# Kernel optimization log

Measured on AMD Instinct MI355X. Metric: run time of the kernel, lower is better.

The kernel has to match this reference:

```python
import jax, jax.numpy as jnp
import numpy as np

EPS = 1e-06  # used both as eps and as the F.threshold threshold (mqjs passes eps as th)


def _pair_log_dist_sum(x1, x2, th):
    # dist[i,j] = ||x1_i||^2 + ||x2_j||^2 - 2 x1_i . x2_j  (n x n)
    x1x2 = x1 @ x2.T
    sq1 = jnp.sum(x1 * x1, axis=1)[:, None]
    sq2 = jnp.sum(x2 * x2, axis=1)[None, :]
    dist = sq1 + sq2 - 2.0 * x1x2
    # F.threshold(dist, th, 1): values <= th -> 1; then clamp(min=1), sqrt, log, row-sum
    dist = jnp.where(dist > th, dist, 1.0)
    dist = jnp.maximum(dist, 1.0)
    return jnp.sum(0.5 * jnp.log(dist), axis=1)  # log(sqrt(d)) == 0.5*log(d)


def _mqjs(inp, tgt, eps):
    n = inp.shape[0]
    x1 = inp.reshape(n, -1)
    x2 = tgt.reshape(n, -1)
    p = (x1 + x2) / 2.0
    ce = _pair_log_dist_sum(x1, p, eps) + _pair_log_dist_sum(x2, p, eps)
    se = _pair_log_dist_sum(x1, x1, eps) * (n / (n - 1))
    return jnp.mean(ce - se)


def setup_inputs() -> dict:
    key = jax.random.key(0)
    k1, k2 = jax.random.split(key)
    n, d = 8192, 256
    inp = jax.random.normal(k1, (n, d), dtype=jnp.float32)
    tgt = jax.random.normal(k2, (n, d), dtype=jnp.float32)
    return {"input": inp, "target": tgt}


def reference(input, target):
    return _mqjs(input, target, EPS)
```

## Files before the change

kernel.cpp:

```cpp
#include <hip/hip_runtime.h>

#define N 8192
#define D 256
#define BM 128
#define BJ 64
#define JG 8
#define GJ (N / BJ / JG)
#define GI (N / BM)
#define NPART (3 * GI * GJ)

typedef int   i32x4 __attribute__((ext_vector_type(4)));
typedef int   i32x8 __attribute__((ext_vector_type(8)));
typedef float f32x4 __attribute__((ext_vector_type(4)));
typedef float f32x2 __attribute__((ext_vector_type(2)));

__device__ __forceinline__ unsigned pack_fp8x4(float a, float b, float c, float d) {
    unsigned lo = __builtin_amdgcn_cvt_pk_fp8_f32(a, b, 0, false);
    return __builtin_amdgcn_cvt_pk_fp8_f32(c, d, lo, true);
}
__device__ __forceinline__ float dequant_sumsq(unsigned q) {
    const float v0 = __builtin_amdgcn_cvt_f32_fp8(q, 0);
    const float v1 = __builtin_amdgcn_cvt_f32_fp8(q, 1);
    const float v2 = __builtin_amdgcn_cvt_f32_fp8(q, 2);
    const float v3 = __builtin_amdgcn_cvt_f32_fp8(q, 3);
    return fmaf(v0, v0, fmaf(v1, v1, fmaf(v2, v2, v3 * v3)));
}

__global__ void prep_kernel(const float* __restrict__ x1, const float* __restrict__ x2,
                            unsigned* __restrict__ x1q, unsigned* __restrict__ x2q,
                            unsigned* __restrict__ pq,
                            float* __restrict__ sq1, float* __restrict__ sq2,
                            float* __restrict__ sqp) {
    const int tid = threadIdx.x, lane = tid & 63, wv = tid >> 6;
    const int row = blockIdx.x * 4 + wv;
    const size_t eb = (size_t)row * D + lane * 4;
    const float4 a = *(const float4*)(x1 + eb);
    const float4 b = *(const float4*)(x2 + eb);
    const float px = 0.5f * (a.x + b.x), py = 0.5f * (a.y + b.y);
    const float pz = 0.5f * (a.z + b.z), pw = 0.5f * (a.w + b.w);
    const unsigned qa = pack_fp8x4(a.x, a.y, a.z, a.w);
    const unsigned qb = pack_fp8x4(b.x, b.y, b.z, b.w);
    const unsigned qp = pack_fp8x4(px, py, pz, pw);
    const size_t wb = (size_t)row * (D / 4) + lane;
    x1q[wb] = qa; x2q[wb] = qb; pq[wb] = qp;
    float s1 = dequant_sumsq(qa), s2 = dequant_sumsq(qb), sp = dequant_sumsq(qp);
    #pragma unroll
    for (int o = 32; o > 0; o >>= 1) {
        s1 += __shfl_down(s1, o, 64);
        s2 += __shfl_down(s2, o, 64);
        sp += __shfl_down(sp, o, 64);
    }
    if (lane == 0) { sq1[row] = s1; sq2[row] = s2; sqp[row] = sp; }
}

__device__ __forceinline__ f32x4 mfma8(i32x8 a, i32x8 b, f32x4 c) {
    return __builtin_amdgcn_mfma_scale_f32_16x16x128_f8f6f4(
        a, b, c, 0, 0, 0, 0x7F7F7F7F, 0, 0x7F7F7F7F);
}

__device__ __forceinline__ i32x8 read_frag(const unsigned char* Ts, int m, int quad) {
    const int r7 = m & 7;
    const i32x4 lo = *(const i32x4*)(Ts + m * 128 + ((((2 * quad)     ^ r7)) << 4));
    const i32x4 hi = *(const i32x4*)(Ts + m * 128 + ((((2 * quad + 1) ^ r7)) << 4));
    i32x8 f;
    f[0] = lo[0]; f[1] = lo[1]; f[2] = lo[2]; f[3] = lo[3];
    f[4] = hi[0]; f[5] = hi[1]; f[6] = hi[2]; f[7] = hi[3];
    return f;
}

__device__ __forceinline__ void stageB8(const unsigned char* __restrict__ g,
                                        unsigned char* s, int rowbase, size_t kb,
                                        int wv, int srow, int sblk) {
    const int row = wv * 8 + srow;
    __builtin_amdgcn_global_load_lds(
        (const __attribute__((address_space(1))) void*)(g + (size_t)(rowbase + row) * D + kb + sblk * 16),
        (__attribute__((address_space(3))) void*)(s + wv * 1024), 16, 0, 0);
}

__device__ __forceinline__ float logsumP(const f32x4 (&acc)[2][2],
                                         const f32x2 (&sa01)[2], const f32x2 (&sa23)[2],
                                         const float sb[2]) {
    float s = 0.0f;
    #pragma unroll
    for (int ti = 0; ti < 2; ++ti) {
        f32x2 pr = {1.0f, 1.0f};
        #pragma unroll
        for (int tj = 0; tj < 2; ++tj) {
            const f32x2 sbv = {sb[tj], sb[tj]};
            const f32x2 t01 = sa01[ti] + sbv, t23 = sa23[ti] + sbv;
            const f32x2 v01 = {acc[ti][tj][0], acc[ti][tj][1]};
            const f32x2 v23 = {acc[ti][tj][2], acc[ti][tj][3]};
            f32x2 d01 = t01 - 2.0f * v01;
            f32x2 d23 = t23 - 2.0f * v23;
            d01 = __builtin_elementwise_max(d01, (f32x2){1.0f, 1.0f});
            d23 = __builtin_elementwise_max(d23, (f32x2){1.0f, 1.0f});
            pr *= d01; pr *= d23;
        }
        s += __log2f(pr.x * pr.y);
    }
    return s;
}

__device__ __forceinline__ float logsumStraddle(const f32x4 (&acc)[2][2],
                                                const f32x2 (&sa01)[2], const f32x2 (&sa23)[2],
                                                const float sb[2],
                                                int wr, int wc, int quad, int l15,
                                                int I0, int J0) {
    float s = 0.0f;
    #pragma unroll
    for (int ti = 0; ti < 2; ++ti) {
        #pragma unroll
        for (int tj = 0; tj < 2; ++tj) {
            const int j = J0 + wc * 32 + tj * 16 + l15;
            float pr = 1.0f;
            #pragma unroll
            for (int r = 0; r < 4; ++r) {
                const int i = I0 + wr * 32 + ti * 16 + quad * 4 + r;
                const float sav = (r < 2) ? ((r & 1) ? sa01[ti].y : sa01[ti].x)
                                          : ((r & 1) ? sa23[ti].y : sa23[ti].x);
                float d = fmaf(-2.0f, acc[ti][tj][r], sav + sb[tj]);
                d = fmaxf(d, 1.0f);
                const float t = (j > i) ? d : 1.0f;
                const float u = (j >= i) ? d : 1.0f;
                pr *= t * u;
            }
            s += __log2f(pr);
        }
    }
    return s;
}

__global__ __launch_bounds__(512, 4) void mqjs_main(
    const unsigned char* __restrict__ x1q, const unsigned char* __restrict__ x2q,
    const unsigned char* __restrict__ pq,
    const float* __restrict__ sq1, const float* __restrict__ sq2,
    const float* __restrict__ sqp, float* __restrict__ partials) {

    __shared__ __align__(16) unsigned char Bs[3][2 * BJ * 128];
    __shared__ float red[8];

    const int tid = threadIdx.x;
    const int lane = tid & 63;
    const int wv = tid >> 6;
    const int wr = wv >> 1, wc = wv & 1;
    const int quad = lane >> 4, l15 = lane & 15;
    const int srow = lane >> 3;
    const int sblk = (lane & 7) ^ srow;

    const int z = blockIdx.z;
    const int I0 = blockIdx.y * BM;
    const int jbase = blockIdx.x * JG;
    const int pid = (z * GI + blockIdx.y) * GJ + blockIdx.x;
    const float wse = -(float)N / (float)(N - 1);

    int jj0 = 0;
    if (z == 2) {
        jj0 = 2 * (int)blockIdx.y - jbase;
        if (jj0 < 0) jj0 = 0;
        if (jj0 >= JG) { if (tid == 0) partials[pid] = 0.0f; return; }
    }

    const unsigned char* Ag = (z == 1) ? x2q : x1q;
    const unsigned char* Bg = (z == 2) ? x1q : pq;
    const float* sqAg = (z == 1) ? sq2 : sq1;
    const float* sqBg = (z == 2) ? sq1 : sqp;

    i32x8 af[2][2];
    f32x2 sa01[2], sa23[2];
    #pragma unroll
    for (int ti = 0; ti < 2; ++ti) {
        #pragma unroll
        for (int kc = 0; kc < 2; ++kc) {
            const size_t ro = (size_t)(I0 + wr * 32 + ti * 16 + l15) * D + kc * 128 + quad * 32;
            af[kc][ti] = *(const i32x8*)(Ag + ro);
        }
        const int sbase = I0 + wr * 32 + ti * 16 + quad * 4;
        const float4 sv = *(const float4*)(sqAg + sbase);
        sa01[ti] = (f32x2){sv.x, sv.y};
        sa23[ti] = (f32x2){sv.z, sv.w};
    }

    stageB8(Bg, Bs[0],        (jbase + jj0) * BJ, 0,   wv, srow, sblk);
    stageB8(Bg, Bs[0] + 8192, (jbase + jj0) * BJ, 128, wv, srow, sblk);
    if (jj0 + 1 < JG) {
        stageB8(Bg, Bs[1],        (jbase + jj0 + 1) * BJ, 0,   wv, srow, sblk);
        stageB8(Bg, Bs[1] + 8192, (jbase + jj0 + 1) * BJ, 128, wv, srow, sblk);
    }

    float tsum = 0.0f;
    const f32x4 zero4 = {0.0f, 0.0f, 0.0f, 0.0f};
    int cur = 0;

    for (int jj = jj0; jj < JG; ++jj) {
        const int J0 = (jbase + jj) * BJ;

        if (jj + 1 < JG) asm volatile("s_waitcnt vmcnt(2)" ::: "memory");
        else             asm volatile("s_waitcnt vmcnt(0)" ::: "memory");
        asm volatile("s_barrier" ::: "memory");

        float sb[2];
        sb[0] = sqBg[J0 + wc * 32 + l15];
        sb[1] = sqBg[J0 + wc * 32 + 16 + l15];

        if (jj + 2 < JG) {
            const int b2 = (cur == 0) ? 2 : cur - 1;
            stageB8(Bg, Bs[b2],        (jbase + jj + 2) * BJ, 0,   wv, srow, sblk);
            stageB8(Bg, Bs[b2] + 8192, (jbase + jj + 2) * BJ, 128, wv, srow, sblk);
        }

        i32x8 bfr0[2], bfr1[2];
        #pragma unroll
        for (int tj = 0; tj < 2; ++tj) {
            bfr0[tj] = read_frag(Bs[cur],        wc * 32 + tj * 16 + l15, quad);
            bfr1[tj] = read_frag(Bs[cur] + 8192, wc * 32 + tj * 16 + l15, quad);
        }

        f32x4 acc[2][2];
        __builtin_amdgcn_s_setprio(1);
        #pragma unroll
        for (int ti = 0; ti < 2; ++ti)
            #pragma unroll
            for (int tj = 0; tj < 2; ++tj)
                acc[ti][tj] = mfma8(af[0][ti], bfr0[tj], zero4);
        #pragma unroll
        for (int ti = 0; ti < 2; ++ti)
            #pragma unroll
            for (int tj = 0; tj < 2; ++tj)
                acc[ti][tj] = mfma8(af[1][ti], bfr1[tj], acc[ti][tj]);
        __builtin_amdgcn_s_setprio(0);

        if (z < 2) {
            tsum += 0.5f * logsumP(acc, sa01, sa23, sb);
        } else if (J0 >= I0 + BM) {
            tsum += wse * logsumP(acc, sa01, sa23, sb);
        } else {
            tsum += 0.5f * wse * logsumStraddle(acc, sa01, sa23, sb, wr, wc, quad, l15, I0, J0);
        }

        cur = (cur == 2) ? 0 : cur + 1;
    }

    tsum *= 0.6931471805599453f;
    #pragma unroll
    for (int o = 32; o > 0; o >>= 1) tsum += __shfl_down(tsum, o, 64);
    if (lane == 0) red[wv] = tsum;
    __syncthreads();
    if (tid == 0) {
        float t = 0.0f;
        #pragma unroll
        for (int i = 0; i < 8; ++i) t += red[i];
        partials[pid] = t;
    }
}

__global__ void finalize_kernel(const float* __restrict__ partials, float* __restrict__ out) {
    const int tid = threadIdx.x;
    const float4 v = ((const float4*)partials)[tid];
    double s = (double)v.x + (double)v.y + (double)v.z + (double)v.w;
    #pragma unroll
    for (int o = 32; o > 0; o >>= 1) s += __shfl_down(s, o, 64);
    __shared__ double r[12];
    if ((tid & 63) == 0) r[tid >> 6] = s;
    __syncthreads();
    if (tid == 0) {
        double t = 0.0;
        #pragma unroll
        for (int i = 0; i < 12; ++i) t += r[i];
        out[0] = (float)(t / (double)N);
    }
}

extern "C" void kernel_launch(void* const* d_in, const int* in_sizes, int n_in,
                              void* d_out, int out_size, void* d_ws, size_t ws_size,
                              hipStream_t stream) {
    const float* x1 = (const float*)d_in[0];
    const float* x2 = (const float*)d_in[1];

    char* ws = (char*)d_ws;
    const size_t MBYTES = (size_t)N * D;
    unsigned* x1q = (unsigned*)(ws);
    unsigned* x2q = (unsigned*)(ws + MBYTES);
    unsigned* pq  = (unsigned*)(ws + 2 * MBYTES);
    float* sq1 = (float*)(ws + 3 * MBYTES);
    float* sq2 = (float*)(ws + 3 * MBYTES + (size_t)N * 4);
    float* sqp = (float*)(ws + 3 * MBYTES + (size_t)N * 8);
    float* partials = (float*)(ws + 3 * MBYTES + (size_t)N * 12);

    prep_kernel<<<N / 4, 256, 0, stream>>>(x1, x2, x1q, x2q, pq, sq1, sq2, sqp);
    mqjs_main<<<dim3(GJ, GI, 3), 512, 0, stream>>>(
        (const unsigned char*)x1q, (const unsigned char*)x2q, (const unsigned char*)pq,
        sq1, sq2, sqp, partials);
    finalize_kernel<<<1, 768, 0, stream>>>(partials, (float*)d_out);
}
```

Baseline: 139.5 us.

## Fuse x1·p and x2·p cross terms into one block sharing staged p tiles

```diff
diff --git a/kernel.cpp b/kernel.cpp
--- a/kernel.cpp
+++ b/kernel.cpp
@@ -7,7 +7,7 @@
 #define JG 8
 #define GJ (N / BJ / JG)
 #define GI (N / BM)
-#define NPART (3 * GI * GJ)
+#define NPART (2 * GI * GJ)
 
 typedef int   i32x4 __attribute__((ext_vector_type(4)));
 typedef int   i32x8 __attribute__((ext_vector_type(8)));
@@ -154,30 +154,34 @@
     const float wse = -(float)N / (float)(N - 1);
 
     int jj0 = 0;
-    if (z == 2) {
+    if (z == 1) {
         jj0 = 2 * (int)blockIdx.y - jbase;
         if (jj0 < 0) jj0 = 0;
         if (jj0 >= JG) { if (tid == 0) partials[pid] = 0.0f; return; }
     }
 
-    const unsigned char* Ag = (z == 1) ? x2q : x1q;
-    const unsigned char* Bg = (z == 2) ? x1q : pq;
-    const float* sqAg = (z == 1) ? sq2 : sq1;
-    const float* sqBg = (z == 2) ? sq1 : sqp;
-
-    i32x8 af[2][2];
-    f32x2 sa01[2], sa23[2];
+    const unsigned char* Bg = (z == 1) ? x1q : pq;
+    const float* sqBg = (z == 1) ? sq1 : sqp;
+
+    i32x8 af1[2][2], af2[2][2];
+    f32x2 sa1_01[2], sa1_23[2], sa2_01[2], sa2_23[2];
     #pragma unroll
     for (int ti = 0; ti < 2; ++ti) {
         #pragma unroll
         for (int kc = 0; kc < 2; ++kc) {
             const size_t ro = (size_t)(I0 + wr * 32 + ti * 16 + l15) * D + kc * 128 + quad * 32;
-            af[kc][ti] = *(const i32x8*)(Ag + ro);
+            af1[kc][ti] = *(const i32x8*)(x1q + ro);
+            if (z == 0) af2[kc][ti] = *(const i32x8*)(x2q + ro);
         }
         const int sbase = I0 + wr * 32 + ti * 16 + quad * 4;
-        const float4 sv = *(const float4*)(sqAg + sbase);
-        sa01[ti] = (f32x2){sv.x, sv.y};
-        sa23[ti] = (f32x2){sv.z, sv.w};
+        const float4 s1v = *(const float4*)(sq1 + sbase);
+        sa1_01[ti] = (f32x2){s1v.x, s1v.y};
+        sa1_23[ti] = (f32x2){s1v.z, s1v.w};
+        if (z == 0) {
+            const float4 s2v = *(const float4*)(sq2 + sbase);
+            sa2_01[ti] = (f32x2){s2v.x, s2v.y};
+            sa2_23[ti] = (f32x2){s2v.z, s2v.w};
+        }
     }
 
     stageB8(Bg, Bs[0],        (jbase + jj0) * BJ, 0,   wv, srow, sblk);
@@ -215,26 +219,52 @@
             bfr1[tj] = read_frag(Bs[cur] + 8192, wc * 32 + tj * 16 + l15, quad);
         }
 
-        f32x4 acc[2][2];
-        __builtin_amdgcn_s_setprio(1);
-        #pragma unroll
-        for (int ti = 0; ti < 2; ++ti)
-            #pragma unroll
-            for (int tj = 0; tj < 2; ++tj)
-                acc[ti][tj] = mfma8(af[0][ti], bfr0[tj], zero4);
-        #pragma unroll
-        for (int ti = 0; ti < 2; ++ti)
-            #pragma unroll
-            for (int tj = 0; tj < 2; ++tj)
-                acc[ti][tj] = mfma8(af[1][ti], bfr1[tj], acc[ti][tj]);
-        __builtin_amdgcn_s_setprio(0);
-
-        if (z < 2) {
-            tsum += 0.5f * logsumP(acc, sa01, sa23, sb);
-        } else if (J0 >= I0 + BM) {
-            tsum += wse * logsumP(acc, sa01, sa23, sb);
+        if (z == 0) {
+            f32x4 acc1[2][2], acc2[2][2];
+            __builtin_amdgcn_s_setprio(1);
+            #pragma unroll
+            for (int ti = 0; ti < 2; ++ti)
+                #pragma unroll
+                for (int tj = 0; tj < 2; ++tj)
+                    acc1[ti][tj] = mfma8(af1[0][ti], bfr0[tj], zero4);
+            #pragma unroll
+            for (int ti = 0; ti < 2; ++ti)
+                #pragma unroll
+                for (int tj = 0; tj < 2; ++tj)
+                    acc1[ti][tj] = mfma8(af1[1][ti], bfr1[tj], acc1[ti][tj]);
+            #pragma unroll
+            for (int ti = 0; ti < 2; ++ti)
+                #pragma unroll
+                for (int tj = 0; tj < 2; ++tj)
+                    acc2[ti][tj] = mfma8(af2[0][ti], bfr0[tj], zero4);
+            #pragma unroll
+            for (int ti = 0; ti < 2; ++ti)
+                #pragma unroll
+                for (int tj = 0; tj < 2; ++tj)
+                    acc2[ti][tj] = mfma8(af2[1][ti], bfr1[tj], acc2[ti][tj]);
+            __builtin_amdgcn_s_setprio(0);
+            tsum += 0.5f * (logsumP(acc1, sa1_01, sa1_23, sb)
+                          + logsumP(acc2, sa2_01, sa2_23, sb));
         } else {
-            tsum += 0.5f * wse * logsumStraddle(acc, sa01, sa23, sb, wr, wc, quad, l15, I0, J0);
+            f32x4 acc[2][2];
+            __builtin_amdgcn_s_setprio(1);
+            #pragma unroll
+            for (int ti = 0; ti < 2; ++ti)
+                #pragma unroll
+                for (int tj = 0; tj < 2; ++tj)
+                    acc[ti][tj] = mfma8(af1[0][ti], bfr0[tj], zero4);
+            #pragma unroll
+            for (int ti = 0; ti < 2; ++ti)
+                #pragma unroll
+                for (int tj = 0; tj < 2; ++tj)
+                    acc[ti][tj] = mfma8(af1[1][ti], bfr1[tj], acc[ti][tj]);
+            __builtin_amdgcn_s_setprio(0);
+            if (J0 >= I0 + BM) {
+                tsum += wse * logsumP(acc, sa1_01, sa1_23, sb);
+            } else {
+                tsum += 0.5f * wse * logsumStraddle(acc, sa1_01, sa1_23, sb,
+                                                    wr, wc, quad, l15, I0, J0);
+            }
         }
 
         cur = (cur == 2) ? 0 : cur + 1;
@@ -259,13 +289,13 @@
     double s = (double)v.x + (double)v.y + (double)v.z + (double)v.w;
     #pragma unroll
     for (int o = 32; o > 0; o >>= 1) s += __shfl_down(s, o, 64);
-    __shared__ double r[12];
+    __shared__ double r[8];
     if ((tid & 63) == 0) r[tid >> 6] = s;
     __syncthreads();
     if (tid == 0) {
         double t = 0.0;
         #pragma unroll
-        for (int i = 0; i < 12; ++i) t += r[i];
+        for (int i = 0; i < 8; ++i) t += r[i];
         out[0] = (float)(t / (double)N);
     }
 }
@@ -287,8 +317,8 @@
     float* partials = (float*)(ws + 3 * MBYTES + (size_t)N * 12);
 
     prep_kernel<<<N / 4, 256, 0, stream>>>(x1, x2, x1q, x2q, pq, sq1, sq2, sqp);
-    mqjs_main<<<dim3(GJ, GI, 3), 512, 0, stream>>>(
+    mqjs_main<<<dim3(GJ, GI, 2), 512, 0, stream>>>(
         (const unsigned char*)x1q, (const unsigned char*)x2q, (const unsigned char*)pq,
         sq1, sq2, sqp, partials);
-    finalize_kernel<<<1, 768, 0, stream>>>(partials, (float*)d_out);
-}
+    finalize_kernel<<<1, 512, 0, stream>>>(partials, (float*)d_out);
+}
```

After: 201.7 us. 1.45x slower.

## Halve j-group per block and preload all B tiles upfront instead of triple-buffering

Applied to the files above, without the earlier changes.

```diff
diff --git a/kernel.cpp b/kernel.cpp
--- a/kernel.cpp
+++ b/kernel.cpp
@@ -4,7 +4,7 @@
 #define D 256
 #define BM 128
 #define BJ 64
-#define JG 8
+#define JG 4
 #define GJ (N / BJ / JG)
 #define GI (N / BM)
 #define NPART (3 * GI * GJ)
@@ -136,7 +136,7 @@
     const float* __restrict__ sq1, const float* __restrict__ sq2,
     const float* __restrict__ sqp, float* __restrict__ partials) {
 
-    __shared__ __align__(16) unsigned char Bs[3][2 * BJ * 128];
+    __shared__ __align__(16) unsigned char Bs[JG][2][8192];
     __shared__ float red[8];
 
     const int tid = threadIdx.x;
@@ -165,6 +165,11 @@
     const float* sqAg = (z == 1) ? sq2 : sq1;
     const float* sqBg = (z == 2) ? sq1 : sqp;
 
+    for (int jj = jj0; jj < JG; ++jj) {
+        stageB8(Bg, &Bs[jj][0][0], (jbase + jj) * BJ, 0,   wv, srow, sblk);
+        stageB8(Bg, &Bs[jj][1][0], (jbase + jj) * BJ, 128, wv, srow, sblk);
+    }
+
     i32x8 af[2][2];
     f32x2 sa01[2], sa23[2];
     #pragma unroll
@@ -180,39 +185,25 @@
         sa23[ti] = (f32x2){sv.z, sv.w};
     }
 
-    stageB8(Bg, Bs[0],        (jbase + jj0) * BJ, 0,   wv, srow, sblk);
-    stageB8(Bg, Bs[0] + 8192, (jbase + jj0) * BJ, 128, wv, srow, sblk);
-    if (jj0 + 1 < JG) {
-        stageB8(Bg, Bs[1],        (jbase + jj0 + 1) * BJ, 0,   wv, srow, sblk);
-        stageB8(Bg, Bs[1] + 8192, (jbase + jj0 + 1) * BJ, 128, wv, srow, sblk);
-    }
+    asm volatile("s_waitcnt vmcnt(0)" ::: "memory");
+    __syncthreads();
 
     float tsum = 0.0f;
     const f32x4 zero4 = {0.0f, 0.0f, 0.0f, 0.0f};
-    int cur = 0;
-
+
+    #pragma unroll 1
     for (int jj = jj0; jj < JG; ++jj) {
         const int J0 = (jbase + jj) * BJ;
-
-        if (jj + 1 < JG) asm volatile("s_waitcnt vmcnt(2)" ::: "memory");
-        else             asm volatile("s_waitcnt vmcnt(0)" ::: "memory");
-        asm volatile("s_barrier" ::: "memory");
 
         float sb[2];
         sb[0] = sqBg[J0 + wc * 32 + l15];
         sb[1] = sqBg[J0 + wc * 32 + 16 + l15];
 
-        if (jj + 2 < JG) {
-            const int b2 = (cur == 0) ? 2 : cur - 1;
-            stageB8(Bg, Bs[b2],        (jbase + jj + 2) * BJ, 0,   wv, srow, sblk);
-            stageB8(Bg, Bs[b2] + 8192, (jbase + jj + 2) * BJ, 128, wv, srow, sblk);
-        }
-
         i32x8 bfr0[2], bfr1[2];
         #pragma unroll
         for (int tj = 0; tj < 2; ++tj) {
-            bfr0[tj] = read_frag(Bs[cur],        wc * 32 + tj * 16 + l15, quad);
-            bfr1[tj] = read_frag(Bs[cur] + 8192, wc * 32 + tj * 16 + l15, quad);
+            bfr0[tj] = read_frag(&Bs[jj][0][0], wc * 32 + tj * 16 + l15, quad);
+            bfr1[tj] = read_frag(&Bs[jj][1][0], wc * 32 + tj * 16 + l15, quad);
         }
 
         f32x4 acc[2][2];
@@ -236,8 +227,6 @@
         } else {
             tsum += 0.5f * wse * logsumStraddle(acc, sa01, sa23, sb, wr, wc, quad, l15, I0, J0);
         }
-
-        cur = (cur == 2) ? 0 : cur + 1;
     }
 
     tsum *= 0.6931471805599453f;
@@ -255,8 +244,10 @@
 
 __global__ void finalize_kernel(const float* __restrict__ partials, float* __restrict__ out) {
     const int tid = threadIdx.x;
-    const float4 v = ((const float4*)partials)[tid];
-    double s = (double)v.x + (double)v.y + (double)v.z + (double)v.w;
+    const float4 a = ((const float4*)partials)[tid];
+    const float4 b = ((const float4*)partials)[tid + 768];
+    double s = (double)a.x + (double)a.y + (double)a.z + (double)a.w
+             + (double)b.x + (double)b.y + (double)b.z + (double)b.w;
     #pragma unroll
     for (int o = 32; o > 0; o >>= 1) s += __shfl_down(s, o, 64);
     __shared__ double r[12];
```

After: 148.7 us. +6.6%, slower.
